# Kernel tuning notes

Hardware: AMD Instinct MI355X
Metric: run time of the kernel (lower is better)

The kernel has to match this reference:

```python
import jax, jax.numpy as jnp
import numpy as np

B, T, H, K = 64, 512, 768, 11
START_ID, END_ID = 9, 10  # tag_to_ix['<CLS>'], tag_to_ix['<SEP>']
NEG = -10000.0


def setup_inputs() -> dict:
    key = jax.random.key(0)
    k1, k2, k3, k4 = jax.random.split(key, 4)
    embeds = jax.random.normal(k1, (B, T, H), dtype=jnp.float32)
    W_fc = jax.random.normal(k2, (K, H), dtype=jnp.float32) * 0.02
    b_fc = jax.random.normal(k3, (K,), dtype=jnp.float32) * 0.02
    transitions = jax.random.normal(k4, (K, K), dtype=jnp.float32)
    # __init__ masking: no transition out of anything into START row, none into END col
    transitions = transitions.at[START_ID, :].set(NEG)
    transitions = transitions.at[:, END_ID].set(NEG)
    return {"embeds": embeds, "W_fc": W_fc, "b_fc": b_fc, "transitions": transitions}


def reference(embeds, W_fc, b_fc, transitions):
    # fc projection: feats[b,t,k] (PLM_crf path: encoder output -> Linear)
    feats = jnp.einsum('bth,kh->btk', embeds, W_fc) + b_fc  # [B,T,K]
    Bv, Tv, Kv = feats.shape

    # Viterbi: log_delta init -10000 except start tag; NOTE the original never
    # adds feats[:, 0] (loop starts at t=1), so we faithfully skip it too.
    log_delta0 = jnp.full((Bv, Kv), NEG, dtype=feats.dtype).at[:, START_ID].set(0.0)

    def step(log_delta, feat_t):
        # transitions[i, j]: score of moving from prev tag j to tag i
        scores = transitions[None, :, :] + log_delta[:, None, :]  # [B,K,K]
        psi_t = jnp.argmax(scores, axis=-1)                       # [B,K] best prev tag
        log_delta_new = jnp.max(scores, axis=-1) + feat_t         # [B,K]
        return log_delta_new, psi_t

    feats_seq = jnp.swapaxes(feats[:, 1:], 0, 1)                  # [T-1,B,K]
    log_delta, psi = jax.lax.scan(step, log_delta0, feats_seq)    # psi: [T-1,B,K]

    score = jnp.max(log_delta, axis=-1)                           # [B]
    last_tag = jnp.argmax(log_delta, axis=-1)                     # [B]

    # Backtrack: path[t] = psi[t+1][path[t+1]] for t = T-2 .. 0
    def back(next_tag, psi_t):
        tag = jnp.take_along_axis(psi_t, next_tag[:, None], axis=-1)[:, 0]
        return tag, tag

    _, path_rest = jax.lax.scan(back, last_tag, psi, reverse=True)  # [T-1,B]
    path = jnp.concatenate([jnp.swapaxes(path_rest, 0, 1), last_tag[:, None]], axis=1)  # [B,T]
    return score, path
```

## Files before the change

kernel.cpp:

```cpp
#include <hip/hip_runtime.h>

#define BB 64
#define TT 512
#define HH 768
#define KK 11
#define START_ID 9
#define NEGV -10000.0f

typedef float vf2 __attribute__((ext_vector_type(2)));

template <int CTRL>
__device__ __forceinline__ float dpp_add(float x) {
    int yi = __builtin_amdgcn_update_dpp(0, __float_as_int(x), CTRL, 0xF, 0xF, false);
    return x + __int_as_float(yi);
}

__device__ __forceinline__ float wave_sum_to_lane63(float x) {
    x = dpp_add<0x111>(x);
    x = dpp_add<0x112>(x);
    x = dpp_add<0x114>(x);
    x = dpp_add<0x118>(x);
    x = dpp_add<0x142>(x);
    x = dpp_add<0x143>(x);
    return x;
}

__device__ __forceinline__ float rlane(float v, int l) {
    return __int_as_float(__builtin_amdgcn_readlane(__float_as_int(v), l));
}

__global__ __launch_bounds__(256) void fc_kernel(const float* __restrict__ embeds,
                                                 const float* __restrict__ W,
                                                 const float* __restrict__ bias,
                                                 float* __restrict__ feats) {
    const int lane = threadIdx.x & 63;
    const int wave_id = (blockIdx.x * blockDim.x + threadIdx.x) >> 6;

    float4 wf[KK][3];
#pragma unroll
    for (int k = 0; k < KK; ++k)
#pragma unroll
        for (int r = 0; r < 3; ++r)
            wf[k][r] = *reinterpret_cast<const float4*>(W + k * HH + r * 256 + lane * 4);

    float bk[KK];
#pragma unroll
    for (int k = 0; k < KK; ++k) bk[k] = bias[k];

    const int base = wave_id * 8;
#pragma unroll 1
    for (int rr = 0; rr < 8; rr += 2) {
        const float* ea = embeds + (size_t)(base + rr) * HH;
        const float* eb = ea + HH;
        float4 a0 = *reinterpret_cast<const float4*>(ea + 0   + lane * 4);
        float4 a1 = *reinterpret_cast<const float4*>(ea + 256 + lane * 4);
        float4 a2 = *reinterpret_cast<const float4*>(ea + 512 + lane * 4);
        float4 b0 = *reinterpret_cast<const float4*>(eb + 0   + lane * 4);
        float4 b1 = *reinterpret_cast<const float4*>(eb + 256 + lane * 4);
        float4 b2 = *reinterpret_cast<const float4*>(eb + 512 + lane * 4);

        vf2 va[6] = {{a0.x, a0.y}, {a0.z, a0.w}, {a1.x, a1.y},
                     {a1.z, a1.w}, {a2.x, a2.y}, {a2.z, a2.w}};
        vf2 vb[6] = {{b0.x, b0.y}, {b0.z, b0.w}, {b1.x, b1.y},
                     {b1.z, b1.w}, {b2.x, b2.y}, {b2.z, b2.w}};

        float rA[KK], rB[KK];
#pragma unroll
        for (int k = 0; k < KK; ++k) {
            vf2 wv[6] = {{wf[k][0].x, wf[k][0].y}, {wf[k][0].z, wf[k][0].w},
                         {wf[k][1].x, wf[k][1].y}, {wf[k][1].z, wf[k][1].w},
                         {wf[k][2].x, wf[k][2].y}, {wf[k][2].z, wf[k][2].w}};
            vf2 sA = va[0] * wv[0];
            vf2 sB = vb[0] * wv[0];
#pragma unroll
            for (int r = 1; r < 6; ++r) { sA += va[r] * wv[r]; sB += vb[r] * wv[r]; }
            rA[k] = wave_sum_to_lane63(sA.x + sA.y);
            rB[k] = wave_sum_to_lane63(sB.x + sB.y);
        }
        if (lane == 63) {
            float* oA = feats + (size_t)(base + rr) * KK;
#pragma unroll
            for (int k = 0; k < KK; ++k) oA[k] = rA[k] + bk[k];
#pragma unroll
            for (int k = 0; k < KK; ++k) oA[KK + k] = rB[k] + bk[k];
        }
    }
}

__global__ __launch_bounds__(256) void viterbi_kernel(const float* __restrict__ feats,
                                                      const float* __restrict__ trans,
                                                      float* __restrict__ out) {
    __shared__ __align__(16) float feats_lds[(TT + 4) * KK];
    __shared__ __align__(16) float dh[(TT - 1) * 12];
    __shared__ int psi_lds[(TT - 1) * KK];
    __shared__ float tr_lds[KK * KK];
    __shared__ int comp[15 * KK];
    __shared__ int bt[16];
    __shared__ int sh_last;

    const int tid = threadIdx.x;
    const int b = blockIdx.x;

    {
        const float4* src = reinterpret_cast<const float4*>(feats + (size_t)b * TT * KK);
        float4* dst = reinterpret_cast<float4*>(feats_lds);
        for (int i = tid; i < TT * KK / 4; i += 256) dst[i] = src[i];
        if (tid < KK * KK) tr_lds[tid] = trans[tid];
    }
    __syncthreads();

    if (tid < 64) {
        const int i = tid;
        const int ci = (i < KK) ? i : 0;
        float tr[KK];
#pragma unroll
        for (int j = 0; j < KK; ++j) tr[j] = (i < KK) ? tr_lds[i * KK + j] : NEGV;

        float delta = (i == START_ID) ? 0.0f : NEGV;

        auto vstep = [&](int t, float fcur) {
            if (i < KK) dh[(t - 1) * 12 + i] = delta;
            float dj[KK];
#pragma unroll
            for (int j = 0; j < KK; ++j) dj[j] = rlane(delta, j);
            float s[KK];
#pragma unroll
            for (int j = 0; j < KK; ++j) s[j] = tr[j] + dj[j];
            float t0 = fmaxf(fmaxf(s[0], s[1]), s[2]);
            float t1 = fmaxf(fmaxf(s[3], s[4]), s[5]);
            float t2 = fmaxf(fmaxf(s[6], s[7]), s[8]);
            float t3 = fmaxf(s[9], s[10]);
            float best = fmaxf(fmaxf(fmaxf(t0, t1), t2), t3);
            delta = best + fcur;
        };

        float fr0 = feats_lds[1 * KK + ci];
        float fr1 = feats_lds[2 * KK + ci];
        float fr2 = feats_lds[3 * KK + ci];
        float fr3 = feats_lds[4 * KK + ci];

        int t = 1;
#pragma unroll 1
        for (; t <= TT - 4; t += 4) {
            vstep(t,     fr0); fr0 = feats_lds[(t + 4) * KK + ci];
            vstep(t + 1, fr1); fr1 = feats_lds[(t + 5) * KK + ci];
            vstep(t + 2, fr2); fr2 = feats_lds[(t + 6) * KK + ci];
            vstep(t + 3, fr3); fr3 = feats_lds[(t + 7) * KK + ci];
        }
        vstep(TT - 3, fr0);
        vstep(TT - 2, fr1);
        vstep(TT - 1, fr2);

        float dfin[KK];
#pragma unroll
        for (int j = 0; j < KK; ++j) dfin[j] = rlane(delta, j);
        float best = dfin[0];
        int last = 0;
#pragma unroll
        for (int j = 1; j < KK; ++j) {
            bool c = dfin[j] > best;
            best = c ? dfin[j] : best;
            last = c ? j : last;
        }
        if (tid == 0) {
            out[b] = best;
            out[BB + (size_t)b * TT + (TT - 1)] = (float)last;
            sh_last = last;
        }
    }
    __syncthreads();

    {
        const int i = tid & 15;
        const int sg = tid >> 4;
        if (i < KK) {
            float tri[KK];
#pragma unroll
            for (int j = 0; j < KK; ++j) tri[j] = tr_lds[i * KK + j];
            for (int s = sg; s < TT - 1; s += 16) {
                const float4* dr = reinterpret_cast<const float4*>(dh + s * 12);
                float4 a = dr[0], c4 = dr[1], d4 = dr[2];
                float sc[KK] = {tri[0] + a.x,  tri[1] + a.y,  tri[2] + a.z,  tri[3] + a.w,
                                tri[4] + c4.x, tri[5] + c4.y, tri[6] + c4.z, tri[7] + c4.w,
                                tri[8] + d4.x, tri[9] + d4.y, tri[10] + d4.z};
                float bv = sc[0];
                int bj = 0;
#pragma unroll
                for (int j = 1; j < KK; ++j) {
                    bool c = sc[j] > bv;
                    bv = c ? sc[j] : bv;
                    bj = c ? j : bj;
                }
                psi_lds[s * KK + i] = bj;
            }
        }
    }
    __syncthreads();

    {
        const int c = tid >> 4;
        const int i = tid & 15;
        if (c < 15 && i < KK) {
            int cur = i;
            for (int s = c * 32 + 31; s >= c * 32; --s) cur = psi_lds[s * KK + cur];
            comp[c * KK + i] = cur;
        } else if (c == 15 && i == 0) {
            int cur = sh_last;
            float* po = out + BB + (size_t)b * TT;
            for (int s = TT - 2; s >= 480; --s) {
                cur = psi_lds[s * KK + cur];
                po[s] = (float)cur;
            }
            bt[15] = cur;
        }
    }
    __syncthreads();

    if (tid == 0) {
        for (int c = 14; c >= 1; --c) bt[c] = comp[c * KK + bt[c + 1]];
    }
    __syncthreads();

    if (tid < 15) {
        const int c = tid;
        int cur = bt[c + 1];
        float* po = out + BB + (size_t)b * TT;
        for (int s = c * 32 + 31; s >= c * 32; --s) {
            cur = psi_lds[s * KK + cur];
            po[s] = (float)cur;
        }
    }
}

extern "C" void kernel_launch(void* const* d_in, const int* in_sizes, int n_in,
                              void* d_out, int out_size, void* d_ws, size_t ws_size,
                              hipStream_t stream) {
    const float* embeds = (const float*)d_in[0];
    const float* W_fc   = (const float*)d_in[1];
    const float* b_fc   = (const float*)d_in[2];
    const float* trans  = (const float*)d_in[3];
    float* out = (float*)d_out;
    float* feats = (float*)d_ws;

    fc_kernel<<<1024, 256, 0, stream>>>(embeds, W_fc, b_fc, feats);
    viterbi_kernel<<<BB, 256, 0, stream>>>(feats, trans, out);
}
```

Measured before the change: 201.5 us.

## Stage FC weights in LDS and software-prefetch next embedding rows

The weight matrix moves from 132 per-thread registers into shared memory (about 33 KB per block) and is streamed back from LDS one tag row ahead. This frees registers so the launch bound can request more waves per CU. The loop also double-buffers the next pair of embedding rows so global loads overlap the dot-product and DPP reductions. The costs are extra LDS traffic and a per-block weight copy. The prefetch on the last iteration wraps around and reloads rows 0-1 of the same 8-row group, which is a wasted load.

```diff
diff --git a/kernel.cpp b/kernel.cpp
--- a/kernel.cpp
+++ b/kernel.cpp
@@ -29,54 +29,86 @@
     return __int_as_float(__builtin_amdgcn_readlane(__float_as_int(v), l));
 }
 
-__global__ __launch_bounds__(256) void fc_kernel(const float* __restrict__ embeds,
-                                                 const float* __restrict__ W,
-                                                 const float* __restrict__ bias,
-                                                 float* __restrict__ feats) {
-    const int lane = threadIdx.x & 63;
-    const int wave_id = (blockIdx.x * blockDim.x + threadIdx.x) >> 6;
-
-    float4 wf[KK][3];
-#pragma unroll
-    for (int k = 0; k < KK; ++k)
-#pragma unroll
-        for (int r = 0; r < 3; ++r)
-            wf[k][r] = *reinterpret_cast<const float4*>(W + k * HH + r * 256 + lane * 4);
+__global__ __launch_bounds__(256, 4) void fc_kernel(const float* __restrict__ embeds,
+                                                    const float* __restrict__ W,
+                                                    const float* __restrict__ bias,
+                                                    float* __restrict__ feats) {
+    __shared__ __align__(16) float w_lds[KK * HH];
+
+    const int tid = threadIdx.x;
+    const int lane = tid & 63;
+
+    {
+        const float4* src = reinterpret_cast<const float4*>(W);
+        float4* dst = reinterpret_cast<float4*>(w_lds);
+#pragma unroll
+        for (int i = 0; i < 9; ++i) {
+            int idx = tid + i * 256;
+            if (idx < KK * HH / 4) dst[idx] = src[idx];
+        }
+    }
 
     float bk[KK];
 #pragma unroll
     for (int k = 0; k < KK; ++k) bk[k] = bias[k];
 
+    __syncthreads();
+
+    const int wave_id = (blockIdx.x * blockDim.x + tid) >> 6;
     const int base = wave_id * 8;
+    const int lo = lane * 4;
+
+    const float* ea = embeds + (size_t)base * HH;
+    const float* eb = ea + HH;
+    float4 a0 = *reinterpret_cast<const float4*>(ea + 0   + lo);
+    float4 a1 = *reinterpret_cast<const float4*>(ea + 256 + lo);
+    float4 a2 = *reinterpret_cast<const float4*>(ea + 512 + lo);
+    float4 b0 = *reinterpret_cast<const float4*>(eb + 0   + lo);
+    float4 b1 = *reinterpret_cast<const float4*>(eb + 256 + lo);
+    float4 b2 = *reinterpret_cast<const float4*>(eb + 512 + lo);
+
 #pragma unroll 1
     for (int rr = 0; rr < 8; rr += 2) {
-        const float* ea = embeds + (size_t)(base + rr) * HH;
-        const float* eb = ea + HH;
-        float4 a0 = *reinterpret_cast<const float4*>(ea + 0   + lane * 4);
-        float4 a1 = *reinterpret_cast<const float4*>(ea + 256 + lane * 4);
-        float4 a2 = *reinterpret_cast<const float4*>(ea + 512 + lane * 4);
-        float4 b0 = *reinterpret_cast<const float4*>(eb + 0   + lane * 4);
-        float4 b1 = *reinterpret_cast<const float4*>(eb + 256 + lane * 4);
-        float4 b2 = *reinterpret_cast<const float4*>(eb + 512 + lane * 4);
+        const int nrr = (rr + 2) & 7;
+        const float* na = embeds + (size_t)(base + nrr) * HH;
+        const float* nb = na + HH;
+        float4 na0 = *reinterpret_cast<const float4*>(na + 0   + lo);
+        float4 na1 = *reinterpret_cast<const float4*>(na + 256 + lo);
+        float4 na2 = *reinterpret_cast<const float4*>(na + 512 + lo);
+        float4 nb0 = *reinterpret_cast<const float4*>(nb + 0   + lo);
+        float4 nb1 = *reinterpret_cast<const float4*>(nb + 256 + lo);
+        float4 nb2 = *reinterpret_cast<const float4*>(nb + 512 + lo);
 
         vf2 va[6] = {{a0.x, a0.y}, {a0.z, a0.w}, {a1.x, a1.y},
                      {a1.z, a1.w}, {a2.x, a2.y}, {a2.z, a2.w}};
         vf2 vb[6] = {{b0.x, b0.y}, {b0.z, b0.w}, {b1.x, b1.y},
                      {b1.z, b1.w}, {b2.x, b2.y}, {b2.z, b2.w}};
 
+        float4 w0 = *reinterpret_cast<const float4*>(w_lds + 0 + lo);
+        float4 w1 = *reinterpret_cast<const float4*>(w_lds + 256 + lo);
+        float4 w2 = *reinterpret_cast<const float4*>(w_lds + 512 + lo);
+
         float rA[KK], rB[KK];
 #pragma unroll
         for (int k = 0; k < KK; ++k) {
-            vf2 wv[6] = {{wf[k][0].x, wf[k][0].y}, {wf[k][0].z, wf[k][0].w},
-                         {wf[k][1].x, wf[k][1].y}, {wf[k][1].z, wf[k][1].w},
-                         {wf[k][2].x, wf[k][2].y}, {wf[k][2].z, wf[k][2].w}};
+            const int nk = (k == KK - 1) ? 0 : k + 1;
+            float4 nw0 = *reinterpret_cast<const float4*>(w_lds + nk * HH + 0 + lo);
+            float4 nw1 = *reinterpret_cast<const float4*>(w_lds + nk * HH + 256 + lo);
+            float4 nw2 = *reinterpret_cast<const float4*>(w_lds + nk * HH + 512 + lo);
+
+            vf2 wv[6] = {{w0.x, w0.y}, {w0.z, w0.w},
+                         {w1.x, w1.y}, {w1.z, w1.w},
+                         {w2.x, w2.y}, {w2.z, w2.w}};
             vf2 sA = va[0] * wv[0];
             vf2 sB = vb[0] * wv[0];
 #pragma unroll
             for (int r = 1; r < 6; ++r) { sA += va[r] * wv[r]; sB += vb[r] * wv[r]; }
             rA[k] = wave_sum_to_lane63(sA.x + sA.y);
             rB[k] = wave_sum_to_lane63(sB.x + sB.y);
-        }
+
+            w0 = nw0; w1 = nw1; w2 = nw2;
+        }
+
         if (lane == 63) {
             float* oA = feats + (size_t)(base + rr) * KK;
 #pragma unroll
@@ -84,6 +116,9 @@
 #pragma unroll
             for (int k = 0; k < KK; ++k) oA[KK + k] = rB[k] + bk[k];
         }
+
+        a0 = na0; a1 = na1; a2 = na2;
+        b0 = nb0; b1 = nb1; b2 = nb2;
     }
 }
 
```

New measurement: 294.7 us. 1.46x slower.
